# Performance work log

Hardware: AMD Instinct MI355X
Metric: run time of the kernel (lower is better)

Reference implementation:

```python
import jax, jax.numpy as jnp
import numpy as np

KERNEL_MUL = 2.0
KERNEL_NUM = 5


def _mmd(source, target):
    n = source.shape[0]
    m = target.shape[0]
    total = jnp.concatenate([source, target], axis=0)  # [n+m, d]
    sq = jnp.sum(total * total, axis=1)  # [n+m]
    l2 = sq[:, None] + sq[None, :] - 2.0 * (total @ total.T)  # [n+m, n+m]
    l2 = jnp.maximum(l2, 0.0)
    n_samples = n + m
    bandwidth = jnp.sum(l2) / (n_samples * n_samples - n_samples)
    bandwidth = bandwidth / (KERNEL_MUL ** (KERNEL_NUM // 2))
    # sum of KERNEL_NUM Gaussian kernels with geometric bandwidths
    kernels = sum(jnp.exp(-l2 / (bandwidth * KERNEL_MUL ** i)) for i in range(KERNEL_NUM))
    b = n  # batch_size = n, as in the torch code
    xx = jnp.sum(kernels[:b, :b]) / (n * n)
    yy = jnp.sum(kernels[b:, b:]) / (m * m)
    xy = jnp.sum(kernels[:b, b:]) / (n * m)
    yx = jnp.sum(kernels[b:, :b]) / (m * n)
    return xx + yy - xy - yx


def setup_inputs() -> dict:
    key = jax.random.key(0)
    k1, k2 = jax.random.split(key)
    source = jax.random.normal(k1, (4096, 256), dtype=jnp.float32)
    target = jax.random.normal(k2, (4096, 256), dtype=jnp.float32)
    return {"source": source, "target": target}


def reference(source, target):
    return _mmd(source, target)
```

## Files before the change

kernel.cpp:

```cpp
#include <hip/hip_runtime.h>
#include <hip/hip_bf16.h>

#define WS_SLOT_OFF   0
#define WS_NEGG_OFF   4096
#define WS_SQPART_OFF 4104
#define WS_CSPART_OFF 5128
#define WS_SQ_OFF     136200
#define WS_G_OFF      168976

#define NROW 8192
#define HALF 4096
#define DIM  256
#define TILE 128
#define NB   64
#define NPAIR (NB * (NB + 1) / 2)
#define GRID_M 512
#define KC   32
#define NC   (DIM / KC)
#define BUFE (TILE * KC)
#define PREPB 128

typedef short  short8 __attribute__((ext_vector_type(8)));
typedef float  f32x4  __attribute__((ext_vector_type(4)));
typedef float  f32x2  __attribute__((ext_vector_type(2)));
typedef unsigned short us4 __attribute__((ext_vector_type(4)));

static __device__ __forceinline__ unsigned short f2bfbits(float f) {
    __hip_bfloat16 h = __float2bfloat16(f);
    return *reinterpret_cast<unsigned short*>(&h);
}
static __device__ __forceinline__ float bfbits2f(unsigned short u) {
    return __uint_as_float(((unsigned int)u) << 16);
}
static __device__ __forceinline__ void gl_lds16(const void* g, void* l) {
    __builtin_amdgcn_global_load_lds(
        (const __attribute__((address_space(1))) void*)g,
        (__attribute__((address_space(3))) void*)l, 16, 0, 0);
}

__global__ __launch_bounds__(256) void k_prep(const float* __restrict__ src,
                                              const float* __restrict__ tgt,
                                              unsigned short* __restrict__ G,
                                              float* __restrict__ sq,
                                              float* __restrict__ cspart,
                                              double* __restrict__ sqpart) {
    __shared__ float cs_lds[4 * 256];
    __shared__ double sq_lds[4];

    int t = threadIdx.x, wid = t >> 6, lane = t & 63;
    int r0 = blockIdx.x * 64;
    int c4 = lane * 4;

    float cs0 = 0.f, cs1 = 0.f, cs2 = 0.f, cs3 = 0.f;
    double wsq = 0.0;
    for (int i = 0; i < 16; ++i) {
        int row = r0 + wid + i * 4;
        const float* base = (row < HALF) ? (src + (size_t)row * DIM)
                                         : (tgt + (size_t)(row - HALF) * DIM);
        float4 v = *(const float4*)(base + c4);
        unsigned short u0 = f2bfbits(v.x), u1 = f2bfbits(v.y),
                       u2 = f2bfbits(v.z), u3 = f2bfbits(v.w);
        us4 uu = {u0, u1, u2, u3};
        *(us4*)(G + (size_t)row * DIM + c4) = uu;
        float r0f = bfbits2f(u0), r1f = bfbits2f(u1),
              r2f = bfbits2f(u2), r3f = bfbits2f(u3);
        cs0 += r0f; cs1 += r1f; cs2 += r2f; cs3 += r3f;
        float s = r0f * r0f + r1f * r1f + r2f * r2f + r3f * r3f;
        #pragma unroll
        for (int off = 32; off; off >>= 1) s += __shfl_down(s, off);
        if (lane == 0) { sq[row] = s; wsq += (double)s; }
    }
    cs_lds[wid * 256 + c4 + 0] = cs0;
    cs_lds[wid * 256 + c4 + 1] = cs1;
    cs_lds[wid * 256 + c4 + 2] = cs2;
    cs_lds[wid * 256 + c4 + 3] = cs3;
    if (lane == 0) sq_lds[wid] = wsq;
    __syncthreads();
    float s = cs_lds[t] + cs_lds[256 + t] + cs_lds[512 + t] + cs_lds[768 + t];
    cspart[blockIdx.x * 256 + t] = s;
    if (t == 0)
        sqpart[blockIdx.x] = sq_lds[0] + sq_lds[1] + sq_lds[2] + sq_lds[3];
}

__global__ __launch_bounds__(256) void k_bw(const float* __restrict__ cspart,
                                            const double* __restrict__ sqpart,
                                            double* __restrict__ negg) {
    __shared__ double red[256];
    __shared__ double red2[256];
    int t = threadIdx.x;
    double c = 0.0;
    for (int b = 0; b < PREPB; ++b) c += (double)cspart[b * 256 + t];
    double s = (t < PREPB) ? sqpart[t] : 0.0;
    red[t]  = s;
    red2[t] = c * c;
    __syncthreads();
    for (int off = 128; off; off >>= 1) {
        if (t < off) { red[t] += red[t + off]; red2[t] += red2[t + off]; }
        __syncthreads();
    }
    if (t == 0) {
        const double N = (double)NROW;
        double sum_l2 = 2.0 * N * red[0] - 2.0 * red2[0];
        double bw = sum_l2 / (N * N - N);
        bw = bw / 4.0;
        negg[0] = -1.4426950408889634 / (16.0 * bw);
    }
}

__global__ __launch_bounds__(256, 2) void k_mmd(const unsigned short* __restrict__ G,
                                                const float* __restrict__ sq,
                                                const double* __restrict__ negg,
                                                double* __restrict__ slots) {
    __shared__ unsigned short As[4 * BUFE];
    __shared__ unsigned short Bs[4 * BUFE];
    __shared__ double wsum[4];

    int bid = blockIdx.x;
    int swz = (bid & 7) * (GRID_M / 8) + (bid >> 3);

    int t = threadIdx.x, wid = t >> 6, lane = t & 63;
    int wr = wid >> 1, wc = wid & 1;
    int rl = lane & 15, klane = lane >> 4;

    int lr0 = wid * 32 + (lane >> 2);
    int slog0 = (lane & 3) ^ ((lr0 >> 1) & 3);
    int lr1 = lr0 + 16;
    int slog1 = (lane & 3) ^ ((lr1 >> 1) & 3);
    size_t ga0 = (size_t)lr0 * DIM + slog0 * 8;
    size_t ga1 = (size_t)lr1 * DIM + slog1 * 8;
    int ld0 = (wid * 32) * KC;
    int ld1 = (wid * 32 + 16) * KC;

    int aoff[4], boff[4];
    #pragma unroll
    for (int f = 0; f < 4; ++f) {
        int ra = wr * 64 + f * 16 + rl;
        aoff[f] = ra * KC + ((klane ^ ((ra >> 1) & 3)) * 8);
        int rb = wc * 64 + f * 16 + rl;
        boff[f] = rb * KC + ((klane ^ ((rb >> 1) & 3)) * 8);
    }

    float ng2 = (float)negg[0];
    float m2g = -2.0f * ng2;
    f32x2 m2g2 = {m2g, m2g};
    int rgrp = lane >> 4;

    double bsum = 0.0;

    #define STAGE(Ab_, Bb_, kcc, buf)                                        \
        do {                                                                 \
            gl_lds16((Ab_) + ga0 + (kcc) * KC, &As[(buf) * BUFE + ld0]);     \
            gl_lds16((Bb_) + ga0 + (kcc) * KC, &Bs[(buf) * BUFE + ld0]);     \
            gl_lds16((Ab_) + ga1 + (kcc) * KC, &As[(buf) * BUFE + ld1]);     \
            gl_lds16((Bb_) + ga1 + (kcc) * KC, &Bs[(buf) * BUFE + ld1]);     \
        } while (0)

    int p = swz;
    int bi = 0, rem = p;
    while (rem >= NB - bi) { rem -= NB - bi; ++bi; }
    int bj = bi + rem;
    const unsigned short* Acur = G + (size_t)bi * TILE * DIM;
    const unsigned short* Bcur = G + (size_t)bj * TILE * DIM;

    STAGE(Acur, Bcur, 0, 0);
    STAGE(Acur, Bcur, 1, 1);

    while (true) {
        int pn = p + GRID_M;
        bool last = (pn >= NPAIR);
        const unsigned short* Anxt = Acur;
        const unsigned short* Bnxt = Bcur;
        int bin = bi, bjn = bj;
        if (!last) {
            int b2 = 0, r2 = pn;
            while (r2 >= NB - b2) { r2 -= NB - b2; ++b2; }
            bin = b2; bjn = b2 + r2;
            Anxt = G + (size_t)bin * TILE * DIM;
            Bnxt = G + (size_t)bjn * TILE * DIM;
        }

        const f32x4 zero4 = {0.f, 0.f, 0.f, 0.f};
        f32x4 acc[4][4];
        #pragma unroll
        for (int i = 0; i < 4; ++i)
            #pragma unroll
            for (int j = 0; j < 4; ++j) acc[i][j] = zero4;

        #pragma unroll
        for (int kc = 0; kc < NC; ++kc) {
            if (kc == NC - 1) {
                if (last) { asm volatile("s_waitcnt vmcnt(0)" ::: "memory"); }
                else      { asm volatile("s_waitcnt vmcnt(4)" ::: "memory"); }
            } else {
                asm volatile("s_waitcnt vmcnt(4)" ::: "memory");
            }
            __builtin_amdgcn_s_barrier();
            __builtin_amdgcn_sched_barrier(0);
            if (kc < NC - 2)   { STAGE(Acur, Bcur, kc + 2, (kc + 2) & 3); }
            else if (!last)    { STAGE(Anxt, Bnxt, kc - 6, (kc + 2) & 3); }

            const unsigned short* Ab = &As[(kc & 3) * BUFE];
            const unsigned short* Bb = &Bs[(kc & 3) * BUFE];
            short8 af[4], bfv[4];
            #pragma unroll
            for (int f = 0; f < 4; ++f) {
                af[f]  = *(const short8*)&Ab[aoff[f]];
                bfv[f] = *(const short8*)&Bb[boff[f]];
            }
            #pragma unroll
            for (int i = 0; i < 4; ++i)
                #pragma unroll
                for (int j = 0; j < 4; ++j)
                    acc[i][j] = __builtin_amdgcn_mfma_f32_16x16x32_bf16(
                        af[i], bfv[j], acc[i][j], 0, 0, 0);
        }

        int gi0 = bi * TILE + wr * 64;
        int gj0 = bj * TILE + wc * 64;

        float sqb4[4];
        #pragma unroll
        for (int j = 0; j < 4; ++j) sqb4[j] = sq[gj0 + j * 16 + rl] * ng2;

        f32x2 tsv = {0.f, 0.f};
        #pragma unroll
        for (int i = 0; i < 4; ++i) {
            int base = gi0 + i * 16 + rgrp * 4;
            f32x2 sa01 = {sq[base + 0] * ng2, sq[base + 1] * ng2};
            f32x2 sa23 = {sq[base + 2] * ng2, sq[base + 3] * ng2};
            #pragma unroll
            for (int j = 0; j < 4; ++j) {
                f32x2 sb = {sqb4[j], sqb4[j]};
                f32x2 x01 = {acc[i][j][0], acc[i][j][1]};
                f32x2 x23 = {acc[i][j][2], acc[i][j][3]};
                x01 = x01 * m2g2 + (sa01 + sb);
                x23 = x23 * m2g2 + (sa23 + sb);
                f32x2 e01, e23;
                e01.x = exp2f(x01.x); e01.y = exp2f(x01.y);
                e23.x = exp2f(x23.x); e23.y = exp2f(x23.y);
                f32x2 p01 = e01 * e01, q01 = p01 * p01,
                      r01 = q01 * q01, s01 = r01 * r01;
                f32x2 p23 = e23 * e23, q23 = p23 * p23,
                      r23 = q23 * q23, s23 = r23 * r23;
                tsv += ((e01 + p01) + (q01 + r01)) + s01;
                tsv += ((e23 + p23) + (q23 + r23)) + s23;
            }
        }
        float tsum = tsv.x + tsv.y;

        float w = ((bi < 32) == (bj < 32)) ? 1.f : -1.f;
        if (bi != bj) w *= 2.f;
        bsum += (double)(tsum * w);

        if (last) break;
        p = pn; bi = bin; bj = bjn; Acur = Anxt; Bcur = Bnxt;
    }
    #undef STAGE

    #pragma unroll
    for (int off = 32; off; off >>= 1) bsum += __shfl_down(bsum, off);
    if (lane == 0) wsum[wid] = bsum;
    __syncthreads();
    if (t == 0)
        slots[bid] = wsum[0] + wsum[1] + wsum[2] + wsum[3];
}

__global__ __launch_bounds__(256) void k_final(const double* __restrict__ slots,
                                               float* __restrict__ out) {
    __shared__ double red[256];
    int t = threadIdx.x;
    double s = slots[t] + slots[t + 256];
    red[t] = s;
    __syncthreads();
    for (int off = 128; off; off >>= 1) {
        if (t < off) red[t] += red[t + off];
        __syncthreads();
    }
    if (t == 0)
        out[0] = (float)(red[0] / ((double)HALF * (double)HALF));
}

extern "C" void kernel_launch(void* const* d_in, const int* in_sizes, int n_in,
                              void* d_out, int out_size, void* d_ws, size_t ws_size,
                              hipStream_t stream) {
    const float* src = (const float*)d_in[0];
    const float* tgt = (const float*)d_in[1];
    float* out = (float*)d_out;

    double* slots     = (double*)((char*)d_ws + WS_SLOT_OFF);
    double* negg      = (double*)((char*)d_ws + WS_NEGG_OFF);
    double* sqpart    = (double*)((char*)d_ws + WS_SQPART_OFF);
    float*  cspart    = (float*)((char*)d_ws + WS_CSPART_OFF);
    float*  sq        = (float*)((char*)d_ws + WS_SQ_OFF);
    unsigned short* G = (unsigned short*)((char*)d_ws + WS_G_OFF);

    k_prep<<<PREPB, 256, 0, stream>>>(src, tgt, G, sq, cspart, sqpart);
    k_bw<<<1, 256, 0, stream>>>(cspart, sqpart, negg);
    k_mmd<<<GRID_M, 256, 0, stream>>>(G, sq, negg, slots);
    k_final<<<1, 256, 0, stream>>>(slots, out);
}
```

Before: 66.67 us.

## Give each wave private LDS tiles and remove block-wide barriers in MMD GEMM loop

Each wave now stages its own 64-row A and B slices into a private, double-buffered LDS region, so the per-k-chunk s_barrier can be dropped and the wave only waits on its own vmcnt. Prefetches are issued after the MFMAs so they refill the buffer just consumed. The final per-block reduction through shared memory and __syncthreads is replaced by per-wave slot writes, and the final kernel now sums 2048 slots. The cost is duplicated global loads: each wave loads its full 64-row A and B slices, and the rows of each tile are loaded by two waves instead of one. LDS use also rises to 64KB per block, which may limit occupancy.

```diff
diff --git a/kernel.cpp b/kernel.cpp
--- a/kernel.cpp
+++ b/kernel.cpp
@@ -2,11 +2,11 @@
 #include <hip/hip_bf16.h>
 
 #define WS_SLOT_OFF   0
-#define WS_NEGG_OFF   4096
-#define WS_SQPART_OFF 4104
-#define WS_CSPART_OFF 5128
-#define WS_SQ_OFF     136200
-#define WS_G_OFF      168976
+#define WS_NEGG_OFF   16384
+#define WS_SQPART_OFF 16392
+#define WS_CSPART_OFF 17416
+#define WS_SQ_OFF     148488
+#define WS_G_OFF      181264
 
 #define NROW 8192
 #define HALF 4096
@@ -17,7 +17,6 @@
 #define GRID_M 512
 #define KC   32
 #define NC   (DIM / KC)
-#define BUFE (TILE * KC)
 #define PREPB 128
 
 typedef short  short8 __attribute__((ext_vector_type(8)));
@@ -111,9 +110,7 @@
                                                 const float* __restrict__ sq,
                                                 const double* __restrict__ negg,
                                                 double* __restrict__ slots) {
-    __shared__ unsigned short As[4 * BUFE];
-    __shared__ unsigned short Bs[4 * BUFE];
-    __shared__ double wsum[4];
+    __shared__ unsigned short lds[4 * 8192];
 
     int bid = blockIdx.x;
     int swz = (bid & 7) * (GRID_M / 8) + (bid >> 3);
@@ -121,23 +118,18 @@
     int t = threadIdx.x, wid = t >> 6, lane = t & 63;
     int wr = wid >> 1, wc = wid & 1;
     int rl = lane & 15, klane = lane >> 4;
-
-    int lr0 = wid * 32 + (lane >> 2);
-    int slog0 = (lane & 3) ^ ((lr0 >> 1) & 3);
-    int lr1 = lr0 + 16;
-    int slog1 = (lane & 3) ^ ((lr1 >> 1) & 3);
-    size_t ga0 = (size_t)lr0 * DIM + slog0 * 8;
-    size_t ga1 = (size_t)lr1 * DIM + slog1 * 8;
-    int ld0 = (wid * 32) * KC;
-    int ld1 = (wid * 32 + 16) * KC;
-
+    int ldsW = wid * 8192;
+
+    int slog = (lane & 3) ^ ((lane >> 3) & 3);
+    size_t gsA = (size_t)(wr * 64 + (lane >> 2)) * DIM + slog * 8;
+    size_t gsB = (size_t)(wc * 64 + (lane >> 2)) * DIM + slog * 8;
+
+    int kswz = (klane ^ ((rl >> 1) & 3)) * 8;
     int aoff[4], boff[4];
     #pragma unroll
     for (int f = 0; f < 4; ++f) {
-        int ra = wr * 64 + f * 16 + rl;
-        aoff[f] = ra * KC + ((klane ^ ((ra >> 1) & 3)) * 8);
-        int rb = wc * 64 + f * 16 + rl;
-        boff[f] = rb * KC + ((klane ^ ((rb >> 1) & 3)) * 8);
+        aoff[f] = f * 512 + rl * 32 + kswz;
+        boff[f] = 2048 + f * 512 + rl * 32 + kswz;
     }
 
     float ng2 = (float)negg[0];
@@ -147,12 +139,15 @@
 
     double bsum = 0.0;
 
-    #define STAGE(Ab_, Bb_, kcc, buf)                                        \
-        do {                                                                 \
-            gl_lds16((Ab_) + ga0 + (kcc) * KC, &As[(buf) * BUFE + ld0]);     \
-            gl_lds16((Bb_) + ga0 + (kcc) * KC, &Bs[(buf) * BUFE + ld0]);     \
-            gl_lds16((Ab_) + ga1 + (kcc) * KC, &As[(buf) * BUFE + ld1]);     \
-            gl_lds16((Bb_) + ga1 + (kcc) * KC, &Bs[(buf) * BUFE + ld1]);     \
+    #define STAGE(Ab_, Bb_, kcc, buf)                                         \
+        do {                                                                  \
+            _Pragma("unroll")                                                 \
+            for (int i_ = 0; i_ < 4; ++i_) {                                  \
+                gl_lds16((Ab_) + gsA + (size_t)i_ * 16 * DIM + (kcc) * KC,    \
+                         &lds[ldsW + (buf) * 4096 + i_ * 512]);               \
+                gl_lds16((Bb_) + gsB + (size_t)i_ * 16 * DIM + (kcc) * KC,    \
+                         &lds[ldsW + (buf) * 4096 + 2048 + i_ * 512]);        \
+            }                                                                 \
         } while (0)
 
     int p = swz;
@@ -188,24 +183,19 @@
 
         #pragma unroll
         for (int kc = 0; kc < NC; ++kc) {
-            if (kc == NC - 1) {
-                if (last) { asm volatile("s_waitcnt vmcnt(0)" ::: "memory"); }
-                else      { asm volatile("s_waitcnt vmcnt(4)" ::: "memory"); }
+            if (kc == NC - 1 && last) {
+                asm volatile("s_waitcnt vmcnt(0)" ::: "memory");
             } else {
-                asm volatile("s_waitcnt vmcnt(4)" ::: "memory");
+                asm volatile("s_waitcnt vmcnt(8)" ::: "memory");
             }
-            __builtin_amdgcn_s_barrier();
             __builtin_amdgcn_sched_barrier(0);
-            if (kc < NC - 2)   { STAGE(Acur, Bcur, kc + 2, (kc + 2) & 3); }
-            else if (!last)    { STAGE(Anxt, Bnxt, kc - 6, (kc + 2) & 3); }
-
-            const unsigned short* Ab = &As[(kc & 3) * BUFE];
-            const unsigned short* Bb = &Bs[(kc & 3) * BUFE];
+
+            const unsigned short* base = &lds[ldsW + (kc & 1) * 4096];
             short8 af[4], bfv[4];
             #pragma unroll
             for (int f = 0; f < 4; ++f) {
-                af[f]  = *(const short8*)&Ab[aoff[f]];
-                bfv[f] = *(const short8*)&Bb[boff[f]];
+                af[f]  = *(const short8*)&base[aoff[f]];
+                bfv[f] = *(const short8*)&base[boff[f]];
             }
             #pragma unroll
             for (int i = 0; i < 4; ++i)
@@ -213,6 +203,10 @@
                 for (int j = 0; j < 4; ++j)
                     acc[i][j] = __builtin_amdgcn_mfma_f32_16x16x32_bf16(
                         af[i], bfv[j], acc[i][j], 0, 0, 0);
+
+            __builtin_amdgcn_sched_barrier(0);
+            if (kc < NC - 2)   { STAGE(Acur, Bcur, kc + 2, kc & 1); }
+            else if (!last)    { STAGE(Anxt, Bnxt, kc - 6, kc & 1); }
         }
 
         int gi0 = bi * TILE + wr * 64;
@@ -225,9 +219,9 @@
         f32x2 tsv = {0.f, 0.f};
         #pragma unroll
         for (int i = 0; i < 4; ++i) {
-            int base = gi0 + i * 16 + rgrp * 4;
-            f32x2 sa01 = {sq[base + 0] * ng2, sq[base + 1] * ng2};
-            f32x2 sa23 = {sq[base + 2] * ng2, sq[base + 3] * ng2};
+            int base2 = gi0 + i * 16 + rgrp * 4;
+            f32x2 sa01 = {sq[base2 + 0] * ng2, sq[base2 + 1] * ng2};
+            f32x2 sa23 = {sq[base2 + 2] * ng2, sq[base2 + 3] * ng2};
             #pragma unroll
             for (int j = 0; j < 4; ++j) {
                 f32x2 sb = {sqb4[j], sqb4[j]};
@@ -259,17 +253,16 @@
 
     #pragma unroll
     for (int off = 32; off; off >>= 1) bsum += __shfl_down(bsum, off);
-    if (lane == 0) wsum[wid] = bsum;
-    __syncthreads();
-    if (t == 0)
-        slots[bid] = wsum[0] + wsum[1] + wsum[2] + wsum[3];
+    if (lane == 0) slots[bid * 4 + wid] = bsum;
 }
 
 __global__ __launch_bounds__(256) void k_final(const double* __restrict__ slots,
                                                float* __restrict__ out) {
     __shared__ double red[256];
     int t = threadIdx.x;
-    double s = slots[t] + slots[t + 256];
+    double s = 0.0;
+    #pragma unroll
+    for (int i = 0; i < 8; ++i) s += slots[t + i * 256];
     red[t] = s;
     __syncthreads();
     for (int off = 128; off; off >>= 1) {
```

After: 76.70 us. 15.0% more time.
